# Performance work log

Hardware: AMD Instinct MI355X
Metric: run time of the kernel (lower is better)

## Reference

```python
import jax, jax.numpy as jnp
import numpy as np

N_NODES = 50000
N_EDGES = 800000
NFEAT, NHID, NCLASS = 512, 64, 40


def setup_inputs() -> dict:
    key = jax.random.key(0)
    ks = jax.random.split(key, 8)
    x = jax.random.normal(ks[0], (N_NODES, NFEAT), dtype=jnp.float32)
    adj_vals = jax.random.uniform(ks[1], (N_EDGES,), dtype=jnp.float32)
    W1 = jax.random.normal(ks[2], (NFEAT, NHID), dtype=jnp.float32) / np.sqrt(NFEAT)
    b1 = jax.random.normal(ks[3], (NHID,), dtype=jnp.float32) * 0.01
    W2 = jax.random.normal(ks[4], (NHID, NCLASS), dtype=jnp.float32) / np.sqrt(NHID)
    b2 = jax.random.normal(ks[5], (NCLASS,), dtype=jnp.float32) * 0.01
    src = jax.random.randint(ks[6], (N_EDGES,), 0, N_NODES, dtype=jnp.int32)
    dst = jax.random.randint(ks[7], (N_EDGES,), 0, N_NODES, dtype=jnp.int32)
    return {"x": x, "adj_vals": adj_vals, "W1": W1, "b1": b1,
            "W2": W2, "b2": b2, "src": src, "dst": dst}


def reference(x, adj_vals, W1, b1, W2, b2, src, dst):
    # GCN forward (quant=False, eval mode => dropout is identity):
    #   h   = relu(adj @ (x @ W1) + b1)
    #   out = adj @ (h @ W2) + b2
    #   return log_softmax(out, dim=1)
    # adj is sparse COO: out[dst] += vals * feats[src]
    n = x.shape[0]

    def spmm(feats):  # [N, d] -> [N, d]
        msgs = adj_vals[:, None] * feats[src]          # [E, d] gather + scale
        return jax.ops.segment_sum(msgs, dst, num_segments=n)

    h = jax.nn.relu(spmm(x @ W1) + b1)                 # [N, nhid]
    out = spmm(h @ W2) + b2                            # [N, nclass]
    return jax.nn.log_softmax(out, axis=1)
```

## Files before the change

kernel.cpp:

```cpp
#include <hip/hip_runtime.h>
#include <math.h>

#define N_NODES 50000
#define N_EDGES 800000
#define NFEAT   512
#define NHID    64
#define NCLASS  40
#define SLOTS   64

#define GEMM_BLOCKS ((N_NODES + 63) / 64)
#define SCAT_BLOCKS (N_EDGES / 256)

typedef __attribute__((ext_vector_type(8))) short bf16x8;
typedef __attribute__((ext_vector_type(4))) float f32x4;

__device__ inline unsigned short f2bf(float f) {
    unsigned int u = __float_as_uint(f);
    u += 0x7FFFu + ((u >> 16) & 1u);
    return (unsigned short)(u >> 16);
}
__device__ inline float bf2f(unsigned short u) {
    return __uint_as_float(((unsigned int)u) << 16);
}
__device__ inline float bflo(unsigned int u) {
    return __uint_as_float(u << 16);
}
__device__ inline float bfhi(unsigned int u) {
    return __uint_as_float(u & 0xFFFF0000u);
}


__global__ __launch_bounds__(256) void init_kernel(int* __restrict__ cursor,
                                                   const float* __restrict__ W1,
                                                   unsigned short* __restrict__ w1t,
                                                   uint4* __restrict__ ev2q) {
    int i = blockIdx.x * blockDim.x + threadIdx.x;
    if (i < N_NODES) cursor[i] = 0;
    if (i < NFEAT * NHID) {
        int k = i >> 6, c = i & 63;
        w1t[(size_t)c * NFEAT + k] = f2bf(W1[i]);
    }
    ev2q[i] = make_uint4(0u, 0u, 0u, 0u);
}

__global__ __launch_bounds__(256) void gemm1_scatter_kernel(
        const float* __restrict__ x,
        const unsigned short* __restrict__ w1t,
        unsigned short* __restrict__ xw,
        const int* __restrict__ dst,
        const int* __restrict__ src,
        const float* __restrict__ adj_vals,
        int* __restrict__ cursor,
        unsigned int* __restrict__ ev2) {
    const int tid = threadIdx.x;
    const unsigned b = blockIdx.x;

    if (b >= GEMM_BLOCKS) {
        const int i = (b - GEMM_BLOCKS) * 256 + tid;
        const int d = dst[i];
        const int p = atomicAdd(&cursor[d], 1);
        if (p < SLOTS)
            ev2[(size_t)d * SLOTS + p] =
                (unsigned int)src[i] | ((unsigned int)f2bf(adj_vals[i]) << 16);
        return;
    }

    const int lane = tid & 63;
    const int wv   = tid >> 6;
    const int i16  = lane & 15;
    const int quad = lane >> 4;

    const int arow = b * 64 + wv * 16 + i16;
    const int arc  = arow < N_NODES ? arow : N_NODES - 1;
    const float* xrow = x + (size_t)arc * NFEAT + quad * 8;
    const unsigned short* wb = w1t + (size_t)i16 * NFEAT + quad * 8;

    f32x4 acc0 = {0.f, 0.f, 0.f, 0.f};
    f32x4 acc1 = acc0, acc2 = acc0, acc3 = acc0;

    float4 pa[4], pb[4];
    bf16x8 bf0[2], bf1[2], bf2[2], bf3[2];

#pragma unroll
    for (int s = 0; s < 4; ++s) {
        pa[s] = *reinterpret_cast<const float4*>(xrow + s * 32);
        pb[s] = *reinterpret_cast<const float4*>(xrow + s * 32 + 4);
    }
#pragma unroll
    for (int s = 0; s < 2; ++s) {
        bf0[s] = *reinterpret_cast<const bf16x8*>(wb + 0 * 16 * NFEAT + s * 32);
        bf1[s] = *reinterpret_cast<const bf16x8*>(wb + 1 * 16 * NFEAT + s * 32);
        bf2[s] = *reinterpret_cast<const bf16x8*>(wb + 2 * 16 * NFEAT + s * 32);
        bf3[s] = *reinterpret_cast<const bf16x8*>(wb + 3 * 16 * NFEAT + s * 32);
    }

#pragma unroll
    for (int s = 0; s < 16; ++s) {
        float4 xa = pa[s & 3], xb = pb[s & 3];
        bf16x8 a;
        a[0] = (short)f2bf(xa.x); a[1] = (short)f2bf(xa.y);
        a[2] = (short)f2bf(xa.z); a[3] = (short)f2bf(xa.w);
        a[4] = (short)f2bf(xb.x); a[5] = (short)f2bf(xb.y);
        a[6] = (short)f2bf(xb.z); a[7] = (short)f2bf(xb.w);
        acc0 = __builtin_amdgcn_mfma_f32_16x16x32_bf16(a, bf0[s & 1], acc0, 0, 0, 0);
        acc1 = __builtin_amdgcn_mfma_f32_16x16x32_bf16(a, bf1[s & 1], acc1, 0, 0, 0);
        acc2 = __builtin_amdgcn_mfma_f32_16x16x32_bf16(a, bf2[s & 1], acc2, 0, 0, 0);
        acc3 = __builtin_amdgcn_mfma_f32_16x16x32_bf16(a, bf3[s & 1], acc3, 0, 0, 0);
        if (s + 4 < 16) {
            pa[s & 3] = *reinterpret_cast<const float4*>(xrow + (s + 4) * 32);
            pb[s & 3] = *reinterpret_cast<const float4*>(xrow + (s + 4) * 32 + 4);
        }
        if (s + 2 < 16) {
            bf0[s & 1] = *reinterpret_cast<const bf16x8*>(wb + 0 * 16 * NFEAT + (s + 2) * 32);
            bf1[s & 1] = *reinterpret_cast<const bf16x8*>(wb + 1 * 16 * NFEAT + (s + 2) * 32);
            bf2[s & 1] = *reinterpret_cast<const bf16x8*>(wb + 2 * 16 * NFEAT + (s + 2) * 32);
            bf3[s & 1] = *reinterpret_cast<const bf16x8*>(wb + 3 * 16 * NFEAT + (s + 2) * 32);
        }
    }

    const int orow0 = b * 64 + wv * 16 + quad * 4;
#pragma unroll
    for (int reg = 0; reg < 4; ++reg) {
        const int orow = orow0 + reg;
        if (orow < N_NODES) {
            unsigned short* op = xw + (size_t)orow * NHID + i16;
            op[ 0] = f2bf(acc0[reg]);
            op[16] = f2bf(acc1[reg]);
            op[32] = f2bf(acc2[reg]);
            op[48] = f2bf(acc3[reg]);
        }
    }
}

__global__ __launch_bounds__(256) void spmm1_gemm2_kernel(
        const unsigned short* __restrict__ xw,
        const unsigned int* __restrict__ ev2,
        const int* __restrict__ counts,
        const float* __restrict__ b1,
        const float* __restrict__ W2,
        unsigned short* __restrict__ hw) {
    __shared__ float w2lds[NHID * NCLASS];
    __shared__ float hlds[4][NHID];
    const int tid  = threadIdx.x;
    const int lane = tid & 63;
    const int wv   = tid >> 6;
    const int ep   = lane >> 4;
    const int f    = lane & 15;

    for (int idx = tid; idx < NHID * NCLASS; idx += 256) w2lds[idx] = W2[idx];
    __syncthreads();

    const int row = blockIdx.x * 4 + wv;
    int cnt = counts[row];
    if (cnt > SLOTS) cnt = SLOTS;
    const unsigned int* erow = ev2 + (size_t)row * SLOTS;

    float a0 = 0.f, a1 = 0.f, a2 = 0.f, a3 = 0.f;
    for (int i0 = ep * 4; i0 < cnt; i0 += 16) {
        uint4 e4 = *reinterpret_cast<const uint4*>(erow + i0);
        uint2 g0 = *reinterpret_cast<const uint2*>(xw + (size_t)(e4.x & 0xFFFFu) * NHID + f * 4);
        uint2 g1 = *reinterpret_cast<const uint2*>(xw + (size_t)(e4.y & 0xFFFFu) * NHID + f * 4);
        uint2 g2 = *reinterpret_cast<const uint2*>(xw + (size_t)(e4.z & 0xFFFFu) * NHID + f * 4);
        uint2 g3 = *reinterpret_cast<const uint2*>(xw + (size_t)(e4.w & 0xFFFFu) * NHID + f * 4);
        float v0 = bfhi(e4.x), v1 = bfhi(e4.y), v2 = bfhi(e4.z), v3 = bfhi(e4.w);
        a0 = fmaf(v0, bflo(g0.x), a0); a1 = fmaf(v0, bfhi(g0.x), a1);
        a2 = fmaf(v0, bflo(g0.y), a2); a3 = fmaf(v0, bfhi(g0.y), a3);
        a0 = fmaf(v1, bflo(g1.x), a0); a1 = fmaf(v1, bfhi(g1.x), a1);
        a2 = fmaf(v1, bflo(g1.y), a2); a3 = fmaf(v1, bfhi(g1.y), a3);
        a0 = fmaf(v2, bflo(g2.x), a0); a1 = fmaf(v2, bfhi(g2.x), a1);
        a2 = fmaf(v2, bflo(g2.y), a2); a3 = fmaf(v2, bfhi(g2.y), a3);
        a0 = fmaf(v3, bflo(g3.x), a0); a1 = fmaf(v3, bfhi(g3.x), a1);
        a2 = fmaf(v3, bflo(g3.y), a2); a3 = fmaf(v3, bfhi(g3.y), a3);
    }
    a0 += __shfl_xor(a0, 16); a0 += __shfl_xor(a0, 32);
    a1 += __shfl_xor(a1, 16); a1 += __shfl_xor(a1, 32);
    a2 += __shfl_xor(a2, 16); a2 += __shfl_xor(a2, 32);
    a3 += __shfl_xor(a3, 16); a3 += __shfl_xor(a3, 32);

    if (ep == 0) {
        float4 bv = *reinterpret_cast<const float4*>(b1 + f * 4);
        float4 hv;
        hv.x = fmaxf(a0 + bv.x, 0.f);
        hv.y = fmaxf(a1 + bv.y, 0.f);
        hv.z = fmaxf(a2 + bv.z, 0.f);
        hv.w = fmaxf(a3 + bv.w, 0.f);
        *reinterpret_cast<float4*>(&hlds[wv][f * 4]) = hv;
    }

    const int c = lane < NCLASS ? lane : (NCLASS - 1);
    float d = 0.f;
#pragma unroll
    for (int k = 0; k < NHID; ++k)
        d = fmaf(hlds[wv][k], w2lds[k * NCLASS + c], d);
    hw[(size_t)row * 64 + lane] = (lane < NCLASS) ? f2bf(d) : (unsigned short)0;
}

__global__ void spmm2_lsm_kernel(const unsigned short* __restrict__ hw,
                                 const unsigned int* __restrict__ ev2,
                                 const int* __restrict__ counts,
                                 const float* __restrict__ b2,
                                 float* __restrict__ out) {
    const int lane = threadIdx.x & 63;
    const int row  = blockIdx.x * 4 + (threadIdx.x >> 6);
    const int ep   = lane >> 4;
    const int f    = lane & 15;
    int cnt = counts[row];
    if (cnt > SLOTS) cnt = SLOTS;
    const unsigned int* erow = ev2 + (size_t)row * SLOTS;

    float a0 = 0.f, a1 = 0.f, a2 = 0.f, a3 = 0.f;
    for (int i0 = ep * 4; i0 < cnt; i0 += 16) {
        uint4 e4 = *reinterpret_cast<const uint4*>(erow + i0);
        uint2 g0 = *reinterpret_cast<const uint2*>(hw + (size_t)(e4.x & 0xFFFFu) * 64 + f * 4);
        uint2 g1 = *reinterpret_cast<const uint2*>(hw + (size_t)(e4.y & 0xFFFFu) * 64 + f * 4);
        uint2 g2 = *reinterpret_cast<const uint2*>(hw + (size_t)(e4.z & 0xFFFFu) * 64 + f * 4);
        uint2 g3 = *reinterpret_cast<const uint2*>(hw + (size_t)(e4.w & 0xFFFFu) * 64 + f * 4);
        float v0 = bfhi(e4.x), v1 = bfhi(e4.y), v2 = bfhi(e4.z), v3 = bfhi(e4.w);
        a0 = fmaf(v0, bflo(g0.x), a0); a1 = fmaf(v0, bfhi(g0.x), a1);
        a2 = fmaf(v0, bflo(g0.y), a2); a3 = fmaf(v0, bfhi(g0.y), a3);
        a0 = fmaf(v1, bflo(g1.x), a0); a1 = fmaf(v1, bfhi(g1.x), a1);
        a2 = fmaf(v1, bflo(g1.y), a2); a3 = fmaf(v1, bfhi(g1.y), a3);
        a0 = fmaf(v2, bflo(g2.x), a0); a1 = fmaf(v2, bfhi(g2.x), a1);
        a2 = fmaf(v2, bflo(g2.y), a2); a3 = fmaf(v2, bfhi(g2.y), a3);
        a0 = fmaf(v3, bflo(g3.x), a0); a1 = fmaf(v3, bfhi(g3.x), a1);
        a2 = fmaf(v3, bflo(g3.y), a2); a3 = fmaf(v3, bfhi(g3.y), a3);
    }
    a0 += __shfl_xor(a0, 16); a0 += __shfl_xor(a0, 32);
    a1 += __shfl_xor(a1, 16); a1 += __shfl_xor(a1, 32);
    a2 += __shfl_xor(a2, 16); a2 += __shfl_xor(a2, 32);
    a3 += __shfl_xor(a3, 16); a3 += __shfl_xor(a3, 32);

    const bool active = f < 10;
    const int  fb     = active ? f : 9;
    float4 bv = *reinterpret_cast<const float4*>(b2 + fb * 4);
    float l0 = a0 + bv.x, l1 = a1 + bv.y, l2 = a2 + bv.z, l3 = a3 + bv.w;

    float m = active ? fmaxf(fmaxf(l0, l1), fmaxf(l2, l3)) : -INFINITY;
#pragma unroll
    for (int o = 8; o > 0; o >>= 1) m = fmaxf(m, __shfl_xor(m, o));
    float s = active ? (expf(l0 - m) + expf(l1 - m) + expf(l2 - m) + expf(l3 - m)) : 0.f;
#pragma unroll
    for (int o = 8; o > 0; o >>= 1) s += __shfl_xor(s, o);
    const float lse = m + logf(s);

    if (active && ep == 0) {
        float4 o4;
        o4.x = l0 - lse; o4.y = l1 - lse; o4.z = l2 - lse; o4.w = l3 - lse;
        *reinterpret_cast<float4*>(&out[(size_t)row * NCLASS + f * 4]) = o4;
    }
}


extern "C" void kernel_launch(void* const* d_in, const int* in_sizes, int n_in,
                              void* d_out, int out_size, void* d_ws, size_t ws_size,
                              hipStream_t stream) {
    const float* x        = (const float*)d_in[0];
    const float* adj_vals = (const float*)d_in[1];
    const float* W1       = (const float*)d_in[2];
    const float* b1       = (const float*)d_in[3];
    const float* W2       = (const float*)d_in[4];
    const float* b2       = (const float*)d_in[5];
    const int*   src      = (const int*)d_in[6];
    const int*   dst      = (const int*)d_in[7];
    float* out = (float*)d_out;

    const size_t OFF_HW   = 6400000;
    const size_t OFF_CUR  = 12800000;
    const size_t OFF_EV   = 13000000;
    const size_t REQUIRED = OFF_EV + (size_t)N_NODES * SLOTS * 4;
    if (ws_size < REQUIRED) return;

    char* ws = (char*)d_ws;
    unsigned short* xw     = (unsigned short*)(ws);
    unsigned short* hw     = (unsigned short*)(ws + OFF_HW);
    unsigned short* w1t    = (unsigned short*)(ws + OFF_HW);
    int*            cursor = (int*)  (ws + OFF_CUR);
    unsigned int*   ev2    = (unsigned int*)(ws + OFF_EV);

    init_kernel<<<3125, 256, 0, stream>>>(cursor, W1, w1t, (uint4*)ev2);
    gemm1_scatter_kernel<<<GEMM_BLOCKS + SCAT_BLOCKS, 256, 0, stream>>>(
        x, w1t, xw, dst, src, adj_vals, cursor, ev2);
    spmm1_gemm2_kernel<<<N_NODES / 4, 256, 0, stream>>>(xw, ev2, cursor, b1, W2, hw);
    spmm2_lsm_kernel<<<N_NODES / 4, 256, 0, stream>>>(hw, ev2, cursor, b2, out);
}
```

Before: 280.1 us.

## Split GEMM1 K dimension across waves with LDS reduction, 16 rows per block

The GEMM1 part now gives each block 16 rows instead of 64, and the four waves split the 512-wide K dimension into four 128-wide chunks. Partial MFMA accumulators go to shared memory, are summed, and are written as bf16 with a vectorized ushort4 store. This quadruples the number of GEMM blocks to improve parallelism and latency hiding on the memory-bound x read. The cost is an LDS round-trip, a barrier, and each block reloading the full W1 slice for fewer rows.

```diff
diff --git a/kernel.cpp b/kernel.cpp
--- a/kernel.cpp
+++ b/kernel.cpp
@@ -8,7 +8,7 @@
 #define NCLASS  40
 #define SLOTS   64
 
-#define GEMM_BLOCKS ((N_NODES + 63) / 64)
+#define GEMM_BLOCKS (N_NODES / 16)
 #define SCAT_BLOCKS (N_EDGES / 256)
 
 typedef __attribute__((ext_vector_type(8))) short bf16x8;
@@ -52,6 +52,7 @@
         const float* __restrict__ adj_vals,
         int* __restrict__ cursor,
         unsigned int* __restrict__ ev2) {
+    __shared__ float red[4][16][68];
     const int tid = threadIdx.x;
     const unsigned b = blockIdx.x;
 
@@ -69,66 +70,68 @@
     const int wv   = tid >> 6;
     const int i16  = lane & 15;
     const int quad = lane >> 4;
-
-    const int arow = b * 64 + wv * 16 + i16;
-    const int arc  = arow < N_NODES ? arow : N_NODES - 1;
-    const float* xrow = x + (size_t)arc * NFEAT + quad * 8;
-    const unsigned short* wb = w1t + (size_t)i16 * NFEAT + quad * 8;
-
-    f32x4 acc0 = {0.f, 0.f, 0.f, 0.f};
-    f32x4 acc1 = acc0, acc2 = acc0, acc3 = acc0;
+    const int kb   = wv * 128;
+
+    const float* xrow = x + (size_t)(b * 16 + i16) * NFEAT + kb + quad * 8;
+    const unsigned short* wb = w1t + (size_t)i16 * NFEAT + kb + quad * 8;
 
     float4 pa[4], pb[4];
-    bf16x8 bf0[2], bf1[2], bf2[2], bf3[2];
-
 #pragma unroll
     for (int s = 0; s < 4; ++s) {
         pa[s] = *reinterpret_cast<const float4*>(xrow + s * 32);
         pb[s] = *reinterpret_cast<const float4*>(xrow + s * 32 + 4);
     }
-#pragma unroll
-    for (int s = 0; s < 2; ++s) {
-        bf0[s] = *reinterpret_cast<const bf16x8*>(wb + 0 * 16 * NFEAT + s * 32);
-        bf1[s] = *reinterpret_cast<const bf16x8*>(wb + 1 * 16 * NFEAT + s * 32);
-        bf2[s] = *reinterpret_cast<const bf16x8*>(wb + 2 * 16 * NFEAT + s * 32);
-        bf3[s] = *reinterpret_cast<const bf16x8*>(wb + 3 * 16 * NFEAT + s * 32);
-    }
-
-#pragma unroll
-    for (int s = 0; s < 16; ++s) {
-        float4 xa = pa[s & 3], xb = pb[s & 3];
+    bf16x8 bfr[2][4];
+#pragma unroll
+    for (int s = 0; s < 2; ++s)
+#pragma unroll
+        for (int ct = 0; ct < 4; ++ct)
+            bfr[s][ct] = *reinterpret_cast<const bf16x8*>(
+                wb + (size_t)ct * 16 * NFEAT + s * 32);
+
+    f32x4 acc[4];
+#pragma unroll
+    for (int ct = 0; ct < 4; ++ct) acc[ct] = (f32x4){0.f, 0.f, 0.f, 0.f};
+
+#pragma unroll
+    for (int s = 0; s < 4; ++s) {
+        float4 xa = pa[s], xb = pb[s];
         bf16x8 a;
         a[0] = (short)f2bf(xa.x); a[1] = (short)f2bf(xa.y);
         a[2] = (short)f2bf(xa.z); a[3] = (short)f2bf(xa.w);
         a[4] = (short)f2bf(xb.x); a[5] = (short)f2bf(xb.y);
         a[6] = (short)f2bf(xb.z); a[7] = (short)f2bf(xb.w);
-        acc0 = __builtin_amdgcn_mfma_f32_16x16x32_bf16(a, bf0[s & 1], acc0, 0, 0, 0);
-        acc1 = __builtin_amdgcn_mfma_f32_16x16x32_bf16(a, bf1[s & 1], acc1, 0, 0, 0);
-        acc2 = __builtin_amdgcn_mfma_f32_16x16x32_bf16(a, bf2[s & 1], acc2, 0, 0, 0);
-        acc3 = __builtin_amdgcn_mfma_f32_16x16x32_bf16(a, bf3[s & 1], acc3, 0, 0, 0);
-        if (s + 4 < 16) {
-            pa[s & 3] = *reinterpret_cast<const float4*>(xrow + (s + 4) * 32);
-            pb[s & 3] = *reinterpret_cast<const float4*>(xrow + (s + 4) * 32 + 4);
+#pragma unroll
+        for (int ct = 0; ct < 4; ++ct)
+            acc[ct] = __builtin_amdgcn_mfma_f32_16x16x32_bf16(a, bfr[s & 1][ct], acc[ct], 0, 0, 0);
+        if (s + 2 < 4) {
+#pragma unroll
+            for (int ct = 0; ct < 4; ++ct)
+                bfr[s & 1][ct] = *reinterpret_cast<const bf16x8*>(
+                    wb + (size_t)ct * 16 * NFEAT + (s + 2) * 32);
         }
-        if (s + 2 < 16) {
-            bf0[s & 1] = *reinterpret_cast<const bf16x8*>(wb + 0 * 16 * NFEAT + (s + 2) * 32);
-            bf1[s & 1] = *reinterpret_cast<const bf16x8*>(wb + 1 * 16 * NFEAT + (s + 2) * 32);
-            bf2[s & 1] = *reinterpret_cast<const bf16x8*>(wb + 2 * 16 * NFEAT + (s + 2) * 32);
-            bf3[s & 1] = *reinterpret_cast<const bf16x8*>(wb + 3 * 16 * NFEAT + (s + 2) * 32);
-        }
-    }
-
-    const int orow0 = b * 64 + wv * 16 + quad * 4;
-#pragma unroll
-    for (int reg = 0; reg < 4; ++reg) {
-        const int orow = orow0 + reg;
-        if (orow < N_NODES) {
-            unsigned short* op = xw + (size_t)orow * NHID + i16;
-            op[ 0] = f2bf(acc0[reg]);
-            op[16] = f2bf(acc1[reg]);
-            op[32] = f2bf(acc2[reg]);
-            op[48] = f2bf(acc3[reg]);
-        }
+    }
+
+#pragma unroll
+    for (int ct = 0; ct < 4; ++ct)
+#pragma unroll
+        for (int reg = 0; reg < 4; ++reg)
+            red[wv][quad * 4 + reg][ct * 16 + i16] = acc[ct][reg];
+    __syncthreads();
+
+    {
+        const int r  = tid >> 4;
+        const int cq = tid & 15;
+        float4 s0 = *reinterpret_cast<const float4*>(&red[0][r][cq * 4]);
+        float4 s1 = *reinterpret_cast<const float4*>(&red[1][r][cq * 4]);
+        float4 s2 = *reinterpret_cast<const float4*>(&red[2][r][cq * 4]);
+        float4 s3 = *reinterpret_cast<const float4*>(&red[3][r][cq * 4]);
+        ushort4 o;
+        o.x = f2bf(s0.x + s1.x + s2.x + s3.x);
+        o.y = f2bf(s0.y + s1.y + s2.y + s3.y);
+        o.z = f2bf(s0.z + s1.z + s2.z + s3.z);
+        o.w = f2bf(s0.w + s1.w + s2.w + s3.w);
+        *reinterpret_cast<ushort4*>(xw + (size_t)(b * 16 + r) * NHID + cq * 4) = o;
     }
 }
 
```

After: 302.3 us. +7.9%, slower.
